# Kernel optimization log

Measured on AMD Instinct MI355X. Metric: run time of the kernel, lower is better.

## Reference

```python
import jax, jax.numpy as jnp
import numpy as np

QMAX = 127.0
EPS = 1e-08


def setup_inputs() -> dict:
    key = jax.random.key(0)
    k1, k2, k3 = jax.random.split(key, 3)
    x = jax.random.normal(k1, (4, 2048, 4096), dtype=jnp.float32)
    weight = jax.random.normal(k2, (4096, 4096), dtype=jnp.float32) * 0.02
    bias = jax.random.normal(k3, (4096,), dtype=jnp.float32) * 0.02
    return {"x": x, "weight": weight, "bias": bias}


def _quantize_weight_per_row(weight):
    # Int8WeightLinear._q_per_row: per-output-row symmetric absmax scales,
    # scale stored as fp16 (then used as fp32 at runtime).
    w = weight.astype(jnp.float32)
    s = jnp.maximum(jnp.max(jnp.abs(w), axis=1, keepdims=True), EPS) / QMAX  # [out,1]
    q = jnp.clip(jnp.round(w / s), -QMAX, QMAX).astype(jnp.int8)             # [out,in]
    s = s[:, 0].astype(jnp.float16).astype(jnp.float32)                      # [out]
    return q, s


def _quantize_activation_per_row(x2d):
    # _quantize_activation_int8_2d: per-token absmax via max(amax, -amin).
    absmax = jnp.maximum(jnp.max(x2d, axis=1), -jnp.min(x2d, axis=1))
    sc = jnp.maximum(absmax.astype(jnp.float32), EPS) / QMAX                  # [rows]
    q = jnp.clip(jnp.round(x2d.astype(jnp.float32) / sc[:, None]), -QMAX, QMAX).astype(jnp.int8)
    return q, sc


def reference(x, weight, bias):
    w_q, w_s = _quantize_weight_per_row(weight)          # int8 [out,in], fp32 [out]
    x2d = x.reshape(-1, x.shape[-1])                      # [rows, in]
    xq, x_sc = _quantize_activation_per_row(x2d)          # int8 [rows,in], fp32 [rows]
    y = jnp.matmul(xq, w_q.T, preferred_element_type=jnp.int32).astype(jnp.float32)
    y = y * x_sc[:, None] * w_s[None, :]                  # [rows, out]
    out = y.astype(x.dtype).reshape(*x.shape[:-1], weight.shape[0])
    # bias buffer is stored fp16 and cast back to activation dtype
    out = out + bias.astype(jnp.float16).astype(x.dtype)
    return out
```

## Files before the change

### kernel.cpp

```cpp
#include <hip/hip_runtime.h>
#include <hip/hip_fp16.h>

typedef int v4i __attribute__((ext_vector_type(4)));

#define QMAXF 127.0f
#define EPSF 1e-8f

template <bool WEIGHT>
__global__ __launch_bounds__(256) void quant_rows(
    const float* __restrict__ src, signed char* __restrict__ q,
    float* __restrict__ scale, int ncols) {
  const int row = blockIdx.x;
  const int t = threadIdx.x;
  const float4* s4 = (const float4*)(src + (size_t)row * ncols);

  float4 v[4];
  float am = 0.f;
#pragma unroll
  for (int p = 0; p < 4; ++p) {
    v[p] = s4[p * 256 + t];
    am = fmaxf(am, fmaxf(fmaxf(fabsf(v[p].x), fabsf(v[p].y)),
                         fmaxf(fabsf(v[p].z), fabsf(v[p].w))));
  }
#pragma unroll
  for (int off = 32; off > 0; off >>= 1) am = fmaxf(am, __shfl_xor(am, off));
  __shared__ float red[4];
  if ((t & 63) == 0) red[t >> 6] = am;
  __syncthreads();
  am = fmaxf(fmaxf(red[0], red[1]), fmaxf(red[2], red[3]));

  const float s = fmaxf(am, EPSF) / QMAXF;

  uint32_t* qrow = (uint32_t*)(q + (size_t)row * ncols);
#pragma unroll
  for (int p = 0; p < 4; ++p) {
    float fx = fminf(fmaxf(rintf(v[p].x / s), -QMAXF), QMAXF);
    float fy = fminf(fmaxf(rintf(v[p].y / s), -QMAXF), QMAXF);
    float fz = fminf(fmaxf(rintf(v[p].z / s), -QMAXF), QMAXF);
    float fw = fminf(fmaxf(rintf(v[p].w / s), -QMAXF), QMAXF);
    uint32_t packed = ((uint32_t)((int)fx & 0xff)) |
                      ((uint32_t)((int)fy & 0xff) << 8) |
                      ((uint32_t)((int)fz & 0xff) << 16) |
                      ((uint32_t)((int)fw & 0xff) << 24);
    qrow[p * 256 + t] = packed;
  }
  if (t == 0) {
    float so = s;
    if (WEIGHT) so = __half2float(__float2half(s));
    scale[row] = so;
  }
}

__device__ __forceinline__ void gload16(const void* g, void* l) {
  __builtin_amdgcn_global_load_lds(
      (const __attribute__((address_space(1))) void*)g,
      (__attribute__((address_space(3))) void*)l, 16, 0, 0);
}

#define STAGE_A(dst, br0, ktoff)                                            \
  do {                                                                      \
    gload16(Ap + (size_t)((br0) + lr) * K + (ktoff) + scsw,                 \
            (dst) + ((br0) + lr) * 128 + sc);                               \
    gload16(Ap + (size_t)((br0) + 128 + lr) * K + (ktoff) + scsw,           \
            (dst) + ((br0) + 128 + lr) * 128 + sc);                         \
  } while (0)

#define STAGE_B(dst, nh, ktoff)                                             \
  do {                                                                      \
    const int r_ = (nh)*32 + lr + (lr & 32);                                \
    gload16(Bp + (size_t)(r_) * K + (ktoff) + scsw, (dst) + r_ * 128 + sc); \
    gload16(Bp + (size_t)(r_ + 128) * K + (ktoff) + scsw,                   \
            (dst) + (r_ + 128) * 128 + sc);                                 \
  } while (0)

#define PHASE(MH, NH, STAGE_STMT, PRE_BAR_STMT)                             \
  do {                                                                      \
    v4i af[4][2], bf[2][2];                                                 \
    _Pragma("unroll") for (int mi = 0; mi < 4; ++mi)                        \
        _Pragma("unroll") for (int ks = 0; ks < 2; ++ks)                    \
            af[mi][ks] = *(const v4i*)(Ad + (arow + ((MH)*4 + mi) * 16) *   \
                                                128 +                       \
                                       ((ac0 + ks * 64) ^ axor));           \
    _Pragma("unroll") for (int ni = 0; ni < 2; ++ni)                        \
        _Pragma("unroll") for (int ks = 0; ks < 2; ++ks)                    \
            bf[ni][ks] = *(const v4i*)(Bd + (brow + ((NH)*2 + ni) * 16) *   \
                                                128 +                       \
                                       ((ac0 + ks * 64) ^ bxor));           \
    STAGE_STMT;                                                             \
    __builtin_amdgcn_s_barrier();                                           \
    asm volatile("s_waitcnt lgkmcnt(0)" ::: "memory");                      \
    __builtin_amdgcn_sched_barrier(0);                                      \
    __builtin_amdgcn_s_setprio(1);                                          \
    _Pragma("unroll") for (int ks = 0; ks < 2; ++ks)                        \
        _Pragma("unroll") for (int mi = 0; mi < 4; ++mi)                    \
            _Pragma("unroll") for (int ni = 0; ni < 2; ++ni)                \
                acc[(MH)*4 + mi][(NH)*2 + ni] =                             \
                    __builtin_amdgcn_mfma_i32_16x16x64_i8(                  \
                        af[mi][ks], bf[ni][ks],                             \
                        acc[(MH)*4 + mi][(NH)*2 + ni], 0, 0, 0);            \
    __builtin_amdgcn_s_setprio(0);                                          \
    PRE_BAR_STMT;                                                           \
    __builtin_amdgcn_s_barrier();                                           \
  } while (0)

__global__ __launch_bounds__(512, 2) void gemm_i8(
    const signed char* __restrict__ A,
    const signed char* __restrict__ B,
    const float* __restrict__ xsc,
    const float* __restrict__ wsc,
    const float* __restrict__ bias,
    float* __restrict__ out, int M, int N, int K) {
  __shared__ __align__(16) signed char lds[131072];
  signed char* const ldsA = lds;
  signed char* const ldsB = lds + 65536;

  const int tid = threadIdx.x;
  const int lane = tid & 63;
  const int wid = tid >> 6;
  const int wm = wid >> 2;
  const int wn = wid & 3;
  const int bm0 = blockIdx.x * 256;
  const int bn0 = blockIdx.y * 256;

  const signed char* Ap = A + (size_t)bm0 * K;
  const signed char* Bp = B + (size_t)bn0 * K;

  const int lr = tid >> 3;
  const int sc = (tid & 7) << 4;
  const int scsw = sc ^ ((lr & 7) << 4);

  const int arow = wm * 128 + (lane & 15);
  const int brow = wn * 64 + (lane & 15);
  const int ac0 = (lane >> 4) << 4;
  const int axor = (arow & 7) << 4;
  const int bxor = (brow & 7) << 4;

  v4i acc[8][4];
#pragma unroll
  for (int i = 0; i < 8; ++i)
#pragma unroll
    for (int j = 0; j < 4; ++j) acc[i][j] = (v4i){0, 0, 0, 0};

  const int NKT = K >> 7;

  STAGE_A(ldsA, 0, 0);
  STAGE_B(ldsB, 0, 0);
  STAGE_A(ldsA, 64, 0);
  STAGE_B(ldsB, 1, 0);
  STAGE_A(ldsA + 32768, 0, 128);
  STAGE_B(ldsB + 32768, 0, 128);
  asm volatile("s_waitcnt vmcnt(4)" ::: "memory");
  __builtin_amdgcn_sched_barrier(0);
  __builtin_amdgcn_s_barrier();

  for (int kt = 0; kt < NKT; ++kt) {
    const int d = kt & 1;
    const signed char* Ad = ldsA + d * 32768;
    const signed char* Bd = ldsB + d * 32768;
    signed char* const An = ldsA + (d ^ 1) * 32768;
    signed char* const Bn = ldsB + (d ^ 1) * 32768;
    const int ko1 = (kt + 1) << 7;
    const int ko2 = (kt + 2) << 7;

    PHASE(0, 0, if (kt + 1 < NKT) STAGE_A(An, 64, ko1), {});
    PHASE(0, 1, if (kt + 1 < NKT) STAGE_B(Bn, 1, ko1), {});
    PHASE(1, 0, if (kt + 2 < NKT) STAGE_A((signed char*)Ad, 0, ko2), {});
    PHASE(1, 1, if (kt + 2 < NKT) STAGE_B((signed char*)Bd, 0, ko2), {
      if (kt < NKT - 2) {
        asm volatile("s_waitcnt vmcnt(4)" ::: "memory");
      } else {
        asm volatile("s_waitcnt vmcnt(0)" ::: "memory");
      }
      __builtin_amdgcn_sched_barrier(0);
    });
  }

#pragma unroll
  for (int mi = 0; mi < 8; ++mi) {
    const int m0 = bm0 + wm * 128 + mi * 16 + ((lane >> 4) << 2);
    const float4 xs = *(const float4*)&xsc[m0];
    const float xsv[4] = {xs.x, xs.y, xs.z, xs.w};
#pragma unroll
    for (int ni = 0; ni < 4; ++ni) {
      const int n = bn0 + wn * 64 + ni * 16 + (lane & 15);
      const float wsn = wsc[n];
      const float bn_ = __half2float(__float2half(bias[n]));
#pragma unroll
      for (int r = 0; r < 4; ++r) {
        out[(size_t)(m0 + r) * N + n] =
            (float)acc[mi][ni][r] * xsv[r] * wsn + bn_;
      }
    }
  }
}

extern "C" void kernel_launch(void* const* d_in, const int* in_sizes, int n_in,
                              void* d_out, int out_size, void* d_ws,
                              size_t ws_size, hipStream_t stream) {
  const float* x = (const float*)d_in[0];
  const float* w = (const float*)d_in[1];
  const float* bias = (const float*)d_in[2];
  float* out = (float*)d_out;

  const int K = 4096;
  const int Nw = in_sizes[1] / K;
  const int M = in_sizes[0] / K;

  signed char* wq = (signed char*)d_ws;
  signed char* xq = wq + (size_t)Nw * K;
  float* wsc = (float*)(xq + (size_t)M * K);
  float* xsc = wsc + Nw;

  quant_rows<true><<<Nw, 256, 0, stream>>>(w, wq, wsc, K);
  quant_rows<false><<<M, 256, 0, stream>>>(x, xq, xsc, K);

  dim3 g2(M / 256, Nw / 256, 1);
  gemm_i8<<<g2, 512, 0, stream>>>(xq, wq, xsc, wsc, bias, out, M, Nw, K);
}
```

Baseline: 205.6 us.

## Restructure int8 GEMM into a 4-slot K=64 pipeline with register double-buffered fragments

Replaces the two-buffer, four-phase K=128 main loop with a four-slot LDS ring of K=64 stages. Each stage is loaded three steps ahead, and the LDS fragments for the next step are read into a second register set while the current step's MFMAs run. This cuts the barriers per K-step from two to one and overlaps LDS reads with MFMA work, at the cost of more fragment registers. It also hardcodes 64 steps (K=4096) and adds a new 4-row swizzle layout.

```diff
diff --git a/kernel.cpp b/kernel.cpp
--- a/kernel.cpp
+++ b/kernel.cpp
@@ -38,11 +38,10 @@
     float fy = fminf(fmaxf(rintf(v[p].y / s), -QMAXF), QMAXF);
     float fz = fminf(fmaxf(rintf(v[p].z / s), -QMAXF), QMAXF);
     float fw = fminf(fmaxf(rintf(v[p].w / s), -QMAXF), QMAXF);
-    uint32_t packed = ((uint32_t)((int)fx & 0xff)) |
-                      ((uint32_t)((int)fy & 0xff) << 8) |
-                      ((uint32_t)((int)fz & 0xff) << 16) |
-                      ((uint32_t)((int)fw & 0xff) << 24);
-    qrow[p * 256 + t] = packed;
+    qrow[p * 256 + t] = ((uint32_t)((int)fx & 0xff)) |
+                        ((uint32_t)((int)fy & 0xff) << 8) |
+                        ((uint32_t)((int)fz & 0xff) << 16) |
+                        ((uint32_t)((int)fw & 0xff) << 24);
   }
   if (t == 0) {
     float so = s;
@@ -57,50 +56,50 @@
       (__attribute__((address_space(3))) void*)l, 16, 0, 0);
 }
 
-#define STAGE_A(dst, br0, ktoff)                                            \
+#define STAGE(s)                                                            \
   do {                                                                      \
-    gload16(Ap + (size_t)((br0) + lr) * K + (ktoff) + scsw,                 \
-            (dst) + ((br0) + lr) * 128 + sc);                               \
-    gload16(Ap + (size_t)((br0) + 128 + lr) * K + (ktoff) + scsw,           \
-            (dst) + ((br0) + 128 + lr) * 128 + sc);                         \
+    signed char* const rb_ = lds + ((s)&3) * 32768;                         \
+    const int ko_ = (s) << 6;                                               \
+    gload16(gA0 + ko_, rb_ + dst0);                                         \
+    gload16(gA1 + ko_, rb_ + 8192 + dst0);                                  \
+    gload16(gB0 + ko_, rb_ + 16384 + dst0);                                 \
+    gload16(gB1 + ko_, rb_ + 24576 + dst0);                                 \
   } while (0)
 
-#define STAGE_B(dst, nh, ktoff)                                             \
+#define FRAG(AF, BF, s)                                                     \
   do {                                                                      \
-    const int r_ = (nh)*32 + lr + (lr & 32);                                \
-    gload16(Bp + (size_t)(r_) * K + (ktoff) + scsw, (dst) + r_ * 128 + sc); \
-    gload16(Bp + (size_t)(r_ + 128) * K + (ktoff) + scsw,                   \
-            (dst) + (r_ + 128) * 128 + sc);                                 \
+    const signed char* rb_ = lds + ((s)&3) * 32768;                         \
+    const signed char* pa_ = rb_ + aoff;                                    \
+    const signed char* pb_ = rb_ + boff;                                    \
+    _Pragma("unroll") for (int mi = 0; mi < 8; ++mi)                        \
+        AF[mi] = *(const v4i*)(pa_ + mi * 1024);                            \
+    _Pragma("unroll") for (int ni = 0; ni < 4; ++ni)                        \
+        BF[ni] = *(const v4i*)(pb_ + ni * 1024);                            \
   } while (0)
 
-#define PHASE(MH, NH, STAGE_STMT, PRE_BAR_STMT)                             \
+#define MFMA32(AF, BF)                                                      \
+  _Pragma("unroll") for (int mi = 0; mi < 8; ++mi)                          \
+      _Pragma("unroll") for (int ni = 0; ni < 4; ++ni)                      \
+          acc[mi][ni] = __builtin_amdgcn_mfma_i32_16x16x64_i8(              \
+              AF[mi], BF[ni], acc[mi][ni], 0, 0, 0)
+
+#define STEP(s, CA, CB, NA, NB)                                             \
   do {                                                                      \
-    v4i af[4][2], bf[2][2];                                                 \
-    _Pragma("unroll") for (int mi = 0; mi < 4; ++mi)                        \
-        _Pragma("unroll") for (int ks = 0; ks < 2; ++ks)                    \
-            af[mi][ks] = *(const v4i*)(Ad + (arow + ((MH)*4 + mi) * 16) *   \
-                                                128 +                       \
-                                       ((ac0 + ks * 64) ^ axor));           \
-    _Pragma("unroll") for (int ni = 0; ni < 2; ++ni)                        \
-        _Pragma("unroll") for (int ks = 0; ks < 2; ++ks)                    \
-            bf[ni][ks] = *(const v4i*)(Bd + (brow + ((NH)*2 + ni) * 16) *   \
-                                                128 +                       \
-                                       ((ac0 + ks * 64) ^ bxor));           \
-    STAGE_STMT;                                                             \
+    if ((s) + 3 < 64) {                                                     \
+      STAGE((s) + 3);                                                       \
+      asm volatile("s_waitcnt vmcnt(8) lgkmcnt(0)" ::: "memory");           \
+    } else if ((s) == 61) {                                                 \
+      asm volatile("s_waitcnt vmcnt(4) lgkmcnt(0)" ::: "memory");           \
+    } else {                                                                \
+      asm volatile("s_waitcnt vmcnt(0) lgkmcnt(0)" ::: "memory");           \
+    }                                                                       \
+    __builtin_amdgcn_sched_barrier(0);                                      \
     __builtin_amdgcn_s_barrier();                                           \
-    asm volatile("s_waitcnt lgkmcnt(0)" ::: "memory");                      \
     __builtin_amdgcn_sched_barrier(0);                                      \
+    if ((s) + 1 < 64) FRAG(NA, NB, (s) + 1);                                \
     __builtin_amdgcn_s_setprio(1);                                          \
-    _Pragma("unroll") for (int ks = 0; ks < 2; ++ks)                        \
-        _Pragma("unroll") for (int mi = 0; mi < 4; ++mi)                    \
-            _Pragma("unroll") for (int ni = 0; ni < 2; ++ni)                \
-                acc[(MH)*4 + mi][(NH)*2 + ni] =                             \
-                    __builtin_amdgcn_mfma_i32_16x16x64_i8(                  \
-                        af[mi][ks], bf[ni][ks],                             \
-                        acc[(MH)*4 + mi][(NH)*2 + ni], 0, 0, 0);            \
+    MFMA32(CA, CB);                                                         \
     __builtin_amdgcn_s_setprio(0);                                          \
-    PRE_BAR_STMT;                                                           \
-    __builtin_amdgcn_s_barrier();                                           \
   } while (0)
 
 __global__ __launch_bounds__(512, 2) void gemm_i8(
@@ -111,8 +110,6 @@
     const float* __restrict__ bias,
     float* __restrict__ out, int M, int N, int K) {
   __shared__ __align__(16) signed char lds[131072];
-  signed char* const ldsA = lds;
-  signed char* const ldsB = lds + 65536;
 
   const int tid = threadIdx.x;
   const int lane = tid & 63;
@@ -122,18 +119,18 @@
   const int bm0 = blockIdx.x * 256;
   const int bn0 = blockIdx.y * 256;
 
-  const signed char* Ap = A + (size_t)bm0 * K;
-  const signed char* Bp = B + (size_t)bn0 * K;
+  const int srow = tid >> 2;
+  const int sch = tid & 3;
+  const int scsw = (sch << 4) ^ ((srow & 3) << 4);
+  const signed char* gA0 = A + (size_t)(bm0 + srow) * K + scsw;
+  const signed char* gA1 = gA0 + (size_t)128 * K;
+  const signed char* gB0 = B + (size_t)(bn0 + srow) * K + scsw;
+  const signed char* gB1 = gB0 + (size_t)128 * K;
+  const int dst0 = tid << 4;
 
-  const int lr = tid >> 3;
-  const int sc = (tid & 7) << 4;
-  const int scsw = sc ^ ((lr & 7) << 4);
-
-  const int arow = wm * 128 + (lane & 15);
-  const int brow = wn * 64 + (lane & 15);
-  const int ac0 = (lane >> 4) << 4;
-  const int axor = (arow & 7) << 4;
-  const int bxor = (brow & 7) << 4;
+  const int fcol = (((lane >> 4) << 4) ^ ((lane & 3) << 4));
+  const int aoff = (wm * 128 + (lane & 15)) * 64 + fcol;
+  const int boff = 16384 + (wn * 64 + (lane & 15)) * 64 + fcol;
 
   v4i acc[8][4];
 #pragma unroll
@@ -141,38 +138,20 @@
 #pragma unroll
     for (int j = 0; j < 4; ++j) acc[i][j] = (v4i){0, 0, 0, 0};
 
-  const int NKT = K >> 7;
+  v4i afA[8], bfA[4], afB[8], bfB[4];
 
-  STAGE_A(ldsA, 0, 0);
-  STAGE_B(ldsB, 0, 0);
-  STAGE_A(ldsA, 64, 0);
-  STAGE_B(ldsB, 1, 0);
-  STAGE_A(ldsA + 32768, 0, 128);
-  STAGE_B(ldsB + 32768, 0, 128);
-  asm volatile("s_waitcnt vmcnt(4)" ::: "memory");
+  STAGE(0);
+  STAGE(1);
+  STAGE(2);
+  asm volatile("s_waitcnt vmcnt(8) lgkmcnt(0)" ::: "memory");
   __builtin_amdgcn_sched_barrier(0);
   __builtin_amdgcn_s_barrier();
+  __builtin_amdgcn_sched_barrier(0);
+  FRAG(afA, bfA, 0);
 
-  for (int kt = 0; kt < NKT; ++kt) {
-    const int d = kt & 1;
-    const signed char* Ad = ldsA + d * 32768;
-    const signed char* Bd = ldsB + d * 32768;
-    signed char* const An = ldsA + (d ^ 1) * 32768;
-    signed char* const Bn = ldsB + (d ^ 1) * 32768;
-    const int ko1 = (kt + 1) << 7;
-    const int ko2 = (kt + 2) << 7;
-
-    PHASE(0, 0, if (kt + 1 < NKT) STAGE_A(An, 64, ko1), {});
-    PHASE(0, 1, if (kt + 1 < NKT) STAGE_B(Bn, 1, ko1), {});
-    PHASE(1, 0, if (kt + 2 < NKT) STAGE_A((signed char*)Ad, 0, ko2), {});
-    PHASE(1, 1, if (kt + 2 < NKT) STAGE_B((signed char*)Bd, 0, ko2), {
-      if (kt < NKT - 2) {
-        asm volatile("s_waitcnt vmcnt(4)" ::: "memory");
-      } else {
-        asm volatile("s_waitcnt vmcnt(0)" ::: "memory");
-      }
-      __builtin_amdgcn_sched_barrier(0);
-    });
+  for (int s2 = 0; s2 < 64; s2 += 2) {
+    STEP(s2, afA, bfA, afB, bfB);
+    STEP(s2 + 1, afB, bfB, afA, bfA);
   }
 
 #pragma unroll
```

Result: faster. 190.9 us (-7.2%).
